# Performance work log

Hardware: AMD Instinct MI355X
Metric: run time of the kernel (lower is better)

## Reference

```python
import jax, jax.numpy as jnp
import numpy as np

TAU = 0.5  # temperature
W_SCALE = 1.0 / np.sqrt(2048.0)  # keep logits in a sane range (like nn.Linear init)


def setup_inputs() -> dict:
    key = jax.random.key(0)
    k1, k2, k3 = jax.random.split(key, 3)
    B, I, O, N = 8192, 2048, 256, 64
    x = jax.random.normal(k1, (B, I), dtype=jnp.float32)
    W = jax.random.normal(k2, (O, N, I), dtype=jnp.float32) * W_SCALE
    b = jnp.zeros((O, N), dtype=jnp.float32)
    grid = jnp.linspace(-1.0, 1.0, N, dtype=jnp.float32)
    # pre-sampled standard Gumbel noise (reparameterized sampling, fixed for determinism)
    u = jax.random.uniform(k3, (B, O, N), dtype=jnp.float32, minval=1e-6, maxval=1.0 - 1e-6)
    gumbel_noise = -jnp.log(-jnp.log(u))
    return {"x": x, "W": W, "b": b, "grid": grid, "gumbel_noise": gumbel_noise}


def reference(x, W, b, grid, gumbel_noise):
    B = x.shape[0]
    O, N, _ = W.shape
    # per-output-feature linears fused into one GEMM; stack(dim=-1) order -> [B, N, O]
    factors = jnp.einsum('bi,oni->bno', x, W) + b.T  # [B, n_bins, out_features]
    # torch .view(B, out_features, n_bins) on the contiguous stacked tensor == reshape
    factors_logits = factors.reshape(B, O, N)
    # gumbel-softmax sampling (soft), then collapse bins onto the value grid
    y = jax.nn.softmax((factors_logits + gumbel_noise) / TAU, axis=-1)  # [B, O, N]
    encoded = jnp.einsum('bon,n->bo', y, grid)  # [B, out_features]
    return (encoded, factors_logits)
```

## Files before the change

### kernel.cpp

```cpp
#include <hip/hip_runtime.h>
#include <hip/hip_bf16.h>
#include <stdint.h>

typedef __bf16 bf16x8 __attribute__((ext_vector_type(8)));
typedef float f32x4 __attribute__((ext_vector_type(4)));
typedef unsigned short u16x8 __attribute__((ext_vector_type(8)));

#define B_ROWS 8192
#define K_DIM  2048
#define O_DIM  256
#define N_BINS 64
#define J_DIM  (O_DIM * N_BINS)

__device__ __forceinline__ unsigned short f2bf(float f) {
    union { float f; unsigned u; } v; v.f = f;
    unsigned r = (v.u + 0x7fffu + ((v.u >> 16) & 1u)) >> 16;
    return (unsigned short)r;
}

__global__ void cvt_x_kernel(const float* __restrict__ x, unsigned short* __restrict__ xb) {
    int i = (blockIdx.x * 256 + threadIdx.x) * 4;
    float4 v = *(const float4*)(x + i);
    ushort4 o;
    o.x = f2bf(v.x); o.y = f2bf(v.y); o.z = f2bf(v.z); o.w = f2bf(v.w);
    *(ushort4*)(xb + i) = o;
}

__global__ void cvt_w_kernel(const float* __restrict__ W, unsigned short* __restrict__ vb) {
    int bid = blockIdx.x;
    int p   = bid >> 1;
    int i0  = (bid & 1) * 1024 + threadIdx.x * 4;
    int src = (p & (O_DIM - 1)) * (N_BINS * K_DIM) + (p >> 8) * K_DIM + i0;
    float4 v = *(const float4*)(W + src);
    ushort4 o;
    o.x = f2bf(v.x); o.y = f2bf(v.y); o.z = f2bf(v.z); o.w = f2bf(v.w);
    *(ushort4*)(vb + (size_t)p * K_DIM + i0) = o;
}

__device__ __forceinline__ u16x8 pack8(float4 a, float4 b) {
    u16x8 r;
    r[0] = f2bf(a.x); r[1] = f2bf(a.y); r[2] = f2bf(a.z); r[3] = f2bf(a.w);
    r[4] = f2bf(b.x); r[5] = f2bf(b.y); r[6] = f2bf(b.z); r[7] = f2bf(b.w);
    return r;
}

#define GLDS(gsrc, ldst) \
    __builtin_amdgcn_global_load_lds((const __attribute__((address_space(1))) void*)(gsrc), \
                                     (__attribute__((address_space(3))) void*)(ldst), 16, 0, 0)
#define SBAR()   __builtin_amdgcn_s_barrier()
#define WAIT_VM(N) do { asm volatile("s_waitcnt vmcnt(" #N ")" ::: "memory"); } while (0)
#define MFMA(a, b, c) (c) = __builtin_amdgcn_mfma_f32_16x16x32_bf16((a), (b), (c), 0, 0, 0)

#define KTILE_BODY(BUF, STAGE_A, STAGE_B) do {                                          \
    bf16x8 a0_[4], a1_[4], bf_[4];                                                      \
    _Pragma("unroll") for (int n_ = 0; n_ < 4; ++n_)                                    \
        bf_[n_] = *(const bf16x8*)&Bs[BUF][brb + n_ * 16][slot];                        \
    _Pragma("unroll") for (int m_ = 0; m_ < 4; ++m_)                                    \
        a0_[m_] = *(const bf16x8*)&As[BUF][arb + m_ * 16][slot];                        \
    STAGE_A;                                                                            \
    __builtin_amdgcn_s_setprio(1);                                                      \
    _Pragma("unroll") for (int m_ = 0; m_ < 4; ++m_) {                                  \
        MFMA(a0_[m_], bf_[0], acc[m_][0]); MFMA(a0_[m_], bf_[1], acc[m_][1]);           \
        MFMA(a0_[m_], bf_[2], acc[m_][2]); MFMA(a0_[m_], bf_[3], acc[m_][3]);           \
    }                                                                                   \
    __builtin_amdgcn_s_setprio(0);                                                      \
    _Pragma("unroll") for (int m_ = 0; m_ < 4; ++m_)                                    \
        a1_[m_] = *(const bf16x8*)&As[BUF][arb + 64 + m_ * 16][slot];                   \
    STAGE_B;                                                                            \
    __builtin_amdgcn_s_setprio(1);                                                      \
    _Pragma("unroll") for (int m_ = 0; m_ < 4; ++m_) {                                  \
        MFMA(a1_[m_], bf_[0], acc[4 + m_][0]); MFMA(a1_[m_], bf_[1], acc[4 + m_][1]);   \
        MFMA(a1_[m_], bf_[2], acc[4 + m_][2]); MFMA(a1_[m_], bf_[3], acc[4 + m_][3]);   \
    }                                                                                   \
    __builtin_amdgcn_s_setprio(0);                                                      \
} while (0)

__global__ __launch_bounds__(512, 2) void gemm8_kernel(
    const unsigned short* __restrict__ xb,
    const unsigned short* __restrict__ vb,
    const float* __restrict__ bias,
    const float* __restrict__ grid,
    const float* __restrict__ gumbel,
    float* __restrict__ logits,
    float* __restrict__ encoded)
{
    __shared__ __align__(16) unsigned char pool[131072];
    auto As = (unsigned short (*)[256][32])pool;
    auto Bs = (unsigned short (*)[256][32])(pool + 65536);
    float* ep = (float*)pool;

    const int tid  = threadIdx.x;
    const int lane = tid & 63;
    const int wv   = tid >> 6;
    const int wr   = wv >> 2;
    const int wc   = wv & 3;

    const int bid = blockIdx.x;
    const int swz  = (bid & 7) * 256 + (bid >> 3);
    const int bm   = (swz >> 8) * 4 + (swz & 3);
    const int bn   = (swz & 255) >> 2;
    const int row0 = bm * 256;
    const int col0 = bn * 256;

    const int oss = (tid * 16) ^ (tid & 32);
    const int sr  = oss >> 6;
    const int sc  = (oss >> 1) & 31;

    const unsigned short* gA = xb + (size_t)(row0 + sr) * K_DIM + sc;
    const unsigned short* gB = vb + (size_t)(col0 + sr) * K_DIM + sc;

    auto stageA = [&](int k, int b) {
        const unsigned short* g = gA + k * 32;
        unsigned short* l = &As[b][0][0] + wv * 512;
        GLDS(g, l);
        GLDS(g + (size_t)128 * K_DIM, l + 4096);
    };
    auto stageB = [&](int k, int b) {
        const unsigned short* g = gB + k * 32;
        unsigned short* l = &Bs[b][0][0] + wv * 512;
        GLDS(g, l);
        GLDS(g + (size_t)128 * K_DIM, l + 4096);
    };

    const int arb  = wr * 128 + (lane & 15);
    const int brb  = wc * 64 + (lane & 15);
    const int slot = ((lane >> 4) * 8) ^ ((lane & 8) << 1);

    f32x4 acc[8][4];
#pragma unroll
    for (int m = 0; m < 8; ++m)
#pragma unroll
        for (int n = 0; n < 4; ++n)
            acc[m][n] = (f32x4){0.f, 0.f, 0.f, 0.f};

    stageA(0, 0); stageB(0, 0);
    stageA(1, 1); stageB(1, 1);
    stageA(2, 2); stageB(2, 2);

    for (int it = 0; it < 15; ++it) {
        const int kt0 = it * 4;
#pragma unroll
        for (int u = 0; u < 4; ++u) {
            WAIT_VM(8); SBAR();
            KTILE_BODY(u, stageA(kt0 + u + 3, (u + 3) & 3), stageB(kt0 + u + 3, (u + 3) & 3));
        }
    }
    WAIT_VM(8); SBAR(); KTILE_BODY(0, stageA(63, 3), stageB(63, 3));
    WAIT_VM(8); SBAR(); KTILE_BODY(1, (void)0, (void)0);
    WAIT_VM(4); SBAR(); KTILE_BODY(2, (void)0, (void)0);
    WAIT_VM(0); SBAR(); KTILE_BODY(3, (void)0, (void)0);

    SBAR();

    const int lane15 = lane & 15;
    const int hi4    = lane >> 4;

    float biasv[4];
#pragma unroll
    for (int n = 0; n < 4; ++n) {
        const int c = col0 + wc * 64 + n * 16 + lane15;
        biasv[n] = bias[(c & (O_DIM - 1)) * N_BINS + (c >> 8)];
    }
    const float4 gridv = *(const float4*)(grid + lane15 * 4);

#pragma unroll
    for (int h = 0; h < 2; ++h) {
        if (wr == h) {
#pragma unroll
            for (int m = 0; m < 8; ++m)
#pragma unroll
                for (int n = 0; n < 4; ++n) {
                    const int cd = wc * 64 + n * 16 + lane15;
#pragma unroll
                    for (int q = 0; q < 4; ++q) {
                        const int rl = m * 16 + hi4 * 4 + q;
                        ep[rl * 256 + (cd ^ ((rl & 7) << 2))] = acc[m][n][q] + biasv[n];
                    }
                }
        }
        SBAR();

        const int cb = hi4 * 64 + lane15 * 4;
        const float* gptr = gumbel + (size_t)(row0 + h * 128 + wv) * J_DIM + col0 + cb;
        float*       lptr = logits + (size_t)(row0 + h * 128 + wv) * J_DIM + col0 + cb;

        float4 gq[4];
#pragma unroll
        for (int p = 0; p < 4; ++p)
            gq[p] = *(const float4*)(gptr + (size_t)p * 8 * J_DIM);

#pragma unroll
        for (int i = 0; i < 16; ++i) {
            const int r = i * 8 + wv;
            const float4 L = *(const float4*)&ep[r * 256 + (cb ^ ((r & 7) << 2))];
            const float4 G = gq[i & 3];
            if (i < 12)
                gq[i & 3] = *(const float4*)(gptr + (size_t)(i + 4) * 8 * J_DIM);

            float z0 = (L.x + G.x) * 2.0f;
            float z1 = (L.y + G.y) * 2.0f;
            float z2 = (L.z + G.z) * 2.0f;
            float z3 = (L.w + G.w) * 2.0f;
            float gmax = fmaxf(fmaxf(z0, z1), fmaxf(z2, z3));
#pragma unroll
            for (int s = 1; s < 16; s <<= 1) gmax = fmaxf(gmax, __shfl_xor(gmax, s));

            const float e0 = __expf(z0 - gmax), e1 = __expf(z1 - gmax);
            const float e2 = __expf(z2 - gmax), e3 = __expf(z3 - gmax);
            float ss = e0 + e1 + e2 + e3;
            float ds = e0 * gridv.x + e1 * gridv.y + e2 * gridv.z + e3 * gridv.w;
#pragma unroll
            for (int s = 1; s < 16; s <<= 1) {
                ss += __shfl_xor(ss, s);
                ds += __shfl_xor(ds, s);
            }

            *(float4*)(lptr + (size_t)i * 8 * J_DIM) = L;
            if (lane15 == 0)
                encoded[(size_t)(row0 + h * 128 + r) * O_DIM + (col0 >> 6) + hi4] = ds / ss;
        }
        SBAR();
    }
}

__global__ __launch_bounds__(256) void gemm_fb(
    const float* __restrict__ xf,
    const float* __restrict__ Wf,
    const float* __restrict__ bias,
    float* __restrict__ logits)
{
    __shared__ unsigned short Asm_[128 * 32];
    __shared__ unsigned short Bsm_[128 * 32];

    const int tid = threadIdx.x;
    const int bid = blockIdx.x;
    const int swz = (bid & 7) * 1024 + (bid >> 3);
    const int row0 = (swz >> 7) * 128;
    const int col0 = (swz & 127) * 128;

    const int lane = tid & 63;
    const int wid  = tid >> 6;
    const int wr   = wid >> 1;
    const int wc   = wid & 1;

    f32x4 acc[4][4];
#pragma unroll
    for (int m = 0; m < 4; ++m)
#pragma unroll
        for (int n = 0; n < 4; ++n)
            acc[m][n] = (f32x4){0.f, 0.f, 0.f, 0.f};

    const int srow = tid >> 2;
    const int koff = (tid & 3) * 8;
    const int ra0 = row0 + srow, ra1 = row0 + 64 + srow;
    const int rb0 = col0 + srow, rb1 = col0 + 64 + srow;

    unsigned short* la0 = &Asm_[tid * 8];
    unsigned short* la1 = &Asm_[(256 + tid) * 8];
    unsigned short* lb0 = &Bsm_[tid * 8];
    unsigned short* lb1 = &Bsm_[(256 + tid) * 8];

    const float* fa0 = xf + (size_t)ra0 * K_DIM + koff;
    const float* fa1 = xf + (size_t)ra1 * K_DIM + koff;
    const float* fb0 = Wf + (size_t)((rb0 & (O_DIM - 1)) * (N_BINS * K_DIM) + (rb0 >> 8) * K_DIM) + koff;
    const float* fb1 = Wf + (size_t)((rb1 & (O_DIM - 1)) * (N_BINS * K_DIM) + (rb1 >> 8) * K_DIM) + koff;

    const int a_row  = wr * 64 + (lane & 15);
    const int b_row  = wc * 64 + (lane & 15);
    const int k_half = (lane >> 4) * 8;

    for (int kt = 0; kt < K_DIM / 32; ++kt) {
        const int kbase = kt * 32;
        *(u16x8*)la0 = pack8(*(const float4*)(fa0 + kbase), *(const float4*)(fa0 + kbase + 4));
        *(u16x8*)la1 = pack8(*(const float4*)(fa1 + kbase), *(const float4*)(fa1 + kbase + 4));
        *(u16x8*)lb0 = pack8(*(const float4*)(fb0 + kbase), *(const float4*)(fb0 + kbase + 4));
        *(u16x8*)lb1 = pack8(*(const float4*)(fb1 + kbase), *(const float4*)(fb1 + kbase + 4));
        __syncthreads();
        bf16x8 af[4], bg[4];
#pragma unroll
        for (int m = 0; m < 4; ++m) af[m] = *(const bf16x8*)&Asm_[(a_row + m * 16) * 32 + k_half];
#pragma unroll
        for (int n = 0; n < 4; ++n) bg[n] = *(const bf16x8*)&Bsm_[(b_row + n * 16) * 32 + k_half];
#pragma unroll
        for (int m = 0; m < 4; ++m)
#pragma unroll
            for (int n = 0; n < 4; ++n)
                MFMA(af[m], bg[n], acc[m][n]);
        __syncthreads();
    }

    const int r_base = row0 + wr * 64 + (lane >> 4) * 4;
    const int c_base = col0 + wc * 64 + (lane & 15);
#pragma unroll
    for (int n = 0; n < 4; ++n) {
        const int c = c_base + n * 16;
        const float bv = bias[(c & (O_DIM - 1)) * N_BINS + (c >> 8)];
#pragma unroll
        for (int m = 0; m < 4; ++m) {
            const int r = r_base + m * 16;
            float* out = logits + (size_t)r * J_DIM + c;
#pragma unroll
            for (int q = 0; q < 4; ++q)
                out[(size_t)q * J_DIM] = acc[m][n][q] + bv;
        }
    }
}

__global__ void softmax_encode_kernel(
    const float* __restrict__ logits,
    const float* __restrict__ gumbel,
    const float* __restrict__ grid,
    float* __restrict__ encoded)
{
    int t = blockIdx.x * 256 + threadIdx.x;
    int g = t >> 4;
    int l = t & 15;
    size_t base = (size_t)g * 64 + l * 4;
    float4 L = *(const float4*)(logits + base);
    float4 G = *(const float4*)(gumbel + base);
    float4 gr = *(const float4*)(grid + l * 4);

    float z0 = (L.x + G.x) * 2.0f;
    float z1 = (L.y + G.y) * 2.0f;
    float z2 = (L.z + G.z) * 2.0f;
    float z3 = (L.w + G.w) * 2.0f;

    float m = fmaxf(fmaxf(z0, z1), fmaxf(z2, z3));
#pragma unroll
    for (int s = 1; s < 16; s <<= 1) m = fmaxf(m, __shfl_xor(m, s, 16));

    float e0 = __expf(z0 - m), e1 = __expf(z1 - m), e2 = __expf(z2 - m), e3 = __expf(z3 - m);
    float ssum = e0 + e1 + e2 + e3;
    float dsum = e0 * gr.x + e1 * gr.y + e2 * gr.z + e3 * gr.w;
#pragma unroll
    for (int s = 1; s < 16; s <<= 1) {
        ssum += __shfl_xor(ssum, s, 16);
        dsum += __shfl_xor(dsum, s, 16);
    }
    if (l == 0) encoded[g] = dsum / ssum;
}

extern "C" void kernel_launch(void* const* d_in, const int* in_sizes, int n_in,
                              void* d_out, int out_size, void* d_ws, size_t ws_size,
                              hipStream_t stream) {
    const float* x      = (const float*)d_in[0];
    const float* W      = (const float*)d_in[1];
    const float* bias   = (const float*)d_in[2];
    const float* grid   = (const float*)d_in[3];
    const float* gumbel = (const float*)d_in[4];

    float* encoded = (float*)d_out;
    float* logits  = (float*)d_out + (size_t)B_ROWS * O_DIM;

    const size_t xb_bytes = (size_t)B_ROWS * K_DIM * 2;
    const size_t vb_bytes = (size_t)J_DIM * K_DIM * 2;

    if (ws_size >= xb_bytes + vb_bytes) {
        unsigned short* xb = (unsigned short*)d_ws;
        unsigned short* vb = (unsigned short*)((char*)d_ws + xb_bytes);
        cvt_x_kernel<<<(B_ROWS * K_DIM) / 1024, 256, 0, stream>>>(x, xb);
        cvt_w_kernel<<<J_DIM * 2, 256, 0, stream>>>(W, vb);
        gemm8_kernel<<<(B_ROWS / 256) * (J_DIM / 256), 512, 0, stream>>>(
            xb, vb, bias, grid, gumbel, logits, encoded);
    } else {
        gemm_fb<<<(B_ROWS / 128) * (J_DIM / 128), 256, 0, stream>>>(x, W, bias, logits);
        softmax_encode_kernel<<<(B_ROWS * O_DIM * 16) / 256, 256, 0, stream>>>(logits, gumbel, grid, encoded);
    }
}
```

Baseline: 700.4 us.

## Restructure GEMM main loop into 64-wide K double-buffer with 8-wave ping-pong phases

Replaces the 4-deep 32-wide K-tile ring buffer with a 2-stage double buffer of 64-wide K tiles. Each tile is processed in four MFMA phases over quadrants of the accumulator, with barriers and lgkmcnt waits between phases so the waves interleave LDS reads, global-to-LDS staging and MFMA work. The aim is better overlap and fewer LDS fragment reloads per MFMA. In exchange the prefetch depth is shallower (one tile ahead, with a full vmcnt(0) wait each tile), there are many more barriers, and B fragments are reloaded once per tile.

```diff
diff --git a/kernel.cpp b/kernel.cpp
--- a/kernel.cpp
+++ b/kernel.cpp
@@ -49,30 +49,66 @@
                                      (__attribute__((address_space(3))) void*)(ldst), 16, 0, 0)
 #define SBAR()   __builtin_amdgcn_s_barrier()
 #define WAIT_VM(N) do { asm volatile("s_waitcnt vmcnt(" #N ")" ::: "memory"); } while (0)
+#define LGKM0()  do { asm volatile("s_waitcnt lgkmcnt(0)" ::: "memory"); } while (0)
 #define MFMA(a, b, c) (c) = __builtin_amdgcn_mfma_f32_16x16x32_bf16((a), (b), (c), 0, 0, 0)
 
-#define KTILE_BODY(BUF, STAGE_A, STAGE_B) do {                                          \
-    bf16x8 a0_[4], a1_[4], bf_[4];                                                      \
-    _Pragma("unroll") for (int n_ = 0; n_ < 4; ++n_)                                    \
-        bf_[n_] = *(const bf16x8*)&Bs[BUF][brb + n_ * 16][slot];                        \
-    _Pragma("unroll") for (int m_ = 0; m_ < 4; ++m_)                                    \
-        a0_[m_] = *(const bf16x8*)&As[BUF][arb + m_ * 16][slot];                        \
-    STAGE_A;                                                                            \
+#define TILE8(P2, STG_A0, STG_B0, STG_A1, STG_B1, VMW) do {                             \
+    bf16x8 aL[4][2], aH[4][2], bL[2][2], bH[2][2];                                      \
+                                                                               \
+    _Pragma("unroll") for (int m_ = 0; m_ < 4; ++m_)                                    \
+        _Pragma("unroll") for (int k_ = 0; k_ < 2; ++k_)                                \
+            aL[m_][k_] = *(const bf16x8*)&As[(P2) + k_][arb + m_ * 16][slot];           \
+    _Pragma("unroll") for (int n_ = 0; n_ < 2; ++n_)                                    \
+        _Pragma("unroll") for (int k_ = 0; k_ < 2; ++k_)                                \
+            bL[n_][k_] = *(const bf16x8*)&Bs[(P2) + k_][brb + n_ * 16][slot];           \
+    STG_A0; STG_B0;                                                                     \
+    SBAR(); LGKM0();                                                                    \
     __builtin_amdgcn_s_setprio(1);                                                      \
-    _Pragma("unroll") for (int m_ = 0; m_ < 4; ++m_) {                                  \
-        MFMA(a0_[m_], bf_[0], acc[m_][0]); MFMA(a0_[m_], bf_[1], acc[m_][1]);           \
-        MFMA(a0_[m_], bf_[2], acc[m_][2]); MFMA(a0_[m_], bf_[3], acc[m_][3]);           \
-    }                                                                                   \
+    _Pragma("unroll") for (int m_ = 0; m_ < 4; ++m_)                                    \
+        _Pragma("unroll") for (int n_ = 0; n_ < 2; ++n_) {                              \
+            MFMA(aL[m_][0], bL[n_][0], acc[m_][n_]);                                    \
+            MFMA(aL[m_][1], bL[n_][1], acc[m_][n_]);                                    \
+        }                                                                               \
+    __builtin_amdgcn_s_setprio(0); SBAR();                                              \
+                                                                               \
+    _Pragma("unroll") for (int n_ = 0; n_ < 2; ++n_)                                    \
+        _Pragma("unroll") for (int k_ = 0; k_ < 2; ++k_)                                \
+            bH[n_][k_] = *(const bf16x8*)&Bs[(P2) + k_][brb + (n_ + 2) * 16][slot];     \
+    STG_A1; STG_B1;                                                                     \
+    SBAR(); LGKM0();                                                                    \
+    __builtin_amdgcn_s_setprio(1);                                                      \
+    _Pragma("unroll") for (int m_ = 0; m_ < 4; ++m_)                                    \
+        _Pragma("unroll") for (int n_ = 0; n_ < 2; ++n_) {                              \
+            MFMA(aL[m_][0], bH[n_][0], acc[m_][2 + n_]);                                \
+            MFMA(aL[m_][1], bH[n_][1], acc[m_][2 + n_]);                                \
+        }                                                                               \
+    __builtin_amdgcn_s_setprio(0); SBAR();                                              \
+                                                                               \
+    _Pragma("unroll") for (int m_ = 0; m_ < 4; ++m_)                                    \
+        _Pragma("unroll") for (int k_ = 0; k_ < 2; ++k_)                                \
+            aH[m_][k_] = *(const bf16x8*)&As[(P2) + k_][arb + 64 + m_ * 16][slot];      \
+    SBAR(); LGKM0();                                                                    \
+    __builtin_amdgcn_s_setprio(1);                                                      \
+    _Pragma("unroll") for (int m_ = 0; m_ < 4; ++m_)                                    \
+        _Pragma("unroll") for (int n_ = 0; n_ < 2; ++n_) {                              \
+            MFMA(aH[m_][0], bH[n_][0], acc[4 + m_][2 + n_]);                            \
+            MFMA(aH[m_][1], bH[n_][1], acc[4 + m_][2 + n_]);                            \
+        }                                                                               \
+    __builtin_amdgcn_s_setprio(0); SBAR();                                              \
+                                                                               \
+    _Pragma("unroll") for (int n_ = 0; n_ < 2; ++n_)                                    \
+        _Pragma("unroll") for (int k_ = 0; k_ < 2; ++k_)                                \
+            bL[n_][k_] = *(const bf16x8*)&Bs[(P2) + k_][brb + n_ * 16][slot];           \
+    SBAR(); LGKM0();                                                                    \
+    __builtin_amdgcn_s_setprio(1);                                                      \
+    _Pragma("unroll") for (int m_ = 0; m_ < 4; ++m_)                                    \
+        _Pragma("unroll") for (int n_ = 0; n_ < 2; ++n_) {                              \
+            MFMA(aH[m_][0], bL[n_][0], acc[4 + m_][n_]);                                \
+            MFMA(aH[m_][1], bL[n_][1], acc[4 + m_][n_]);                                \
+        }                                                                               \
     __builtin_amdgcn_s_setprio(0);                                                      \
-    _Pragma("unroll") for (int m_ = 0; m_ < 4; ++m_)                                    \
-        a1_[m_] = *(const bf16x8*)&As[BUF][arb + 64 + m_ * 16][slot];                   \
-    STAGE_B;                                                                            \
-    __builtin_amdgcn_s_setprio(1);                                                      \
-    _Pragma("unroll") for (int m_ = 0; m_ < 4; ++m_) {                                  \
-        MFMA(a1_[m_], bf_[0], acc[4 + m_][0]); MFMA(a1_[m_], bf_[1], acc[4 + m_][1]);   \
-        MFMA(a1_[m_], bf_[2], acc[4 + m_][2]); MFMA(a1_[m_], bf_[3], acc[4 + m_][3]);   \
-    }                                                                                   \
-    __builtin_amdgcn_s_setprio(0);                                                      \
+    VMW;                                                                                \
+    SBAR();                                                                             \
 } while (0)
 
 __global__ __launch_bounds__(512, 2) void gemm8_kernel(
@@ -109,17 +145,15 @@
     const unsigned short* gA = xb + (size_t)(row0 + sr) * K_DIM + sc;
     const unsigned short* gB = vb + (size_t)(col0 + sr) * K_DIM + sc;
 
-    auto stageA = [&](int k, int b) {
-        const unsigned short* g = gA + k * 32;
-        unsigned short* l = &As[b][0][0] + wv * 512;
-        GLDS(g, l);
-        GLDS(g + (size_t)128 * K_DIM, l + 4096);
+    auto stA = [&](int kt, int h, int b2) {
+        const unsigned short* g = gA + (size_t)h * 128 * K_DIM + kt * 64;
+        GLDS(g,      &As[b2 + 0][h * 128][0] + wv * 512);
+        GLDS(g + 32, &As[b2 + 1][h * 128][0] + wv * 512);
     };
-    auto stageB = [&](int k, int b) {
-        const unsigned short* g = gB + k * 32;
-        unsigned short* l = &Bs[b][0][0] + wv * 512;
-        GLDS(g, l);
-        GLDS(g + (size_t)128 * K_DIM, l + 4096);
+    auto stB = [&](int kt, int h, int b2) {
+        const unsigned short* g = gB + (size_t)h * 128 * K_DIM + kt * 64;
+        GLDS(g,      &Bs[b2 + 0][h * 128][0] + wv * 512);
+        GLDS(g + 32, &Bs[b2 + 1][h * 128][0] + wv * 512);
     };
 
     const int arb  = wr * 128 + (lane & 15);
@@ -133,22 +167,19 @@
         for (int n = 0; n < 4; ++n)
             acc[m][n] = (f32x4){0.f, 0.f, 0.f, 0.f};
 
-    stageA(0, 0); stageB(0, 0);
-    stageA(1, 1); stageB(1, 1);
-    stageA(2, 2); stageB(2, 2);
+    stA(0, 0, 0); stB(0, 0, 0);
+    stA(0, 1, 0); stB(0, 1, 0);
+    WAIT_VM(0); SBAR();
 
     for (int it = 0; it < 15; ++it) {
-        const int kt0 = it * 4;
-#pragma unroll
-        for (int u = 0; u < 4; ++u) {
-            WAIT_VM(8); SBAR();
-            KTILE_BODY(u, stageA(kt0 + u + 3, (u + 3) & 3), stageB(kt0 + u + 3, (u + 3) & 3));
-        }
-    }
-    WAIT_VM(8); SBAR(); KTILE_BODY(0, stageA(63, 3), stageB(63, 3));
-    WAIT_VM(8); SBAR(); KTILE_BODY(1, (void)0, (void)0);
-    WAIT_VM(4); SBAR(); KTILE_BODY(2, (void)0, (void)0);
-    WAIT_VM(0); SBAR(); KTILE_BODY(3, (void)0, (void)0);
+        const int k2 = it * 2;
+        TILE8(0, stA(k2 + 1, 0, 2), stB(k2 + 1, 0, 2),
+                 stA(k2 + 1, 1, 2), stB(k2 + 1, 1, 2), WAIT_VM(0));
+        TILE8(2, stA(k2 + 2, 0, 0), stB(k2 + 2, 0, 0),
+                 stA(k2 + 2, 1, 0), stB(k2 + 2, 1, 0), WAIT_VM(0));
+    }
+    TILE8(0, stA(31, 0, 2), stB(31, 0, 2), stA(31, 1, 2), stB(31, 1, 2), WAIT_VM(0));
+    TILE8(2, (void)0, (void)0, (void)0, (void)0, (void)0);
 
     SBAR();
 
```

New measurement: 740.8 us. 1.06x slower.
